# Kernel optimization log

Measured on AMD Instinct MI355X. Metric: run time of the kernel, lower is better.

The kernel has to match this reference:

```python
import jax, jax.numpy as jnp
import numpy as np

K = 16  # K_neighbors

def linear_positions(pixels):
    # normalized flat (pixels, 2) grid positions, matching LinearPositions(normalize=True, flat_output=True)
    wd = int(round(pixels ** 0.5))
    h = jnp.repeat(jnp.arange(wd, dtype=jnp.float32)[:, None], wd, axis=1)
    w = jnp.repeat(jnp.arange(wd, dtype=jnp.float32)[None, :], wd, axis=0)
    pos = jnp.stack([h, w], axis=-1) / (wd - 1)
    return pos.reshape(pixels, 2)


def setup_inputs() -> dict:
    key = jax.random.key(0)
    ks = jax.random.split(key, 8)
    B, Wn, P, C = 4, 16, 256, 32
    inp = {
        "x": jax.random.normal(ks[0], (B, Wn, P, C), dtype=jnp.float32),
        "sf_w0": jax.random.normal(ks[1], (3 * K, 128), dtype=jnp.float32) * 0.05,
        "sf_b0": jnp.zeros((128,), jnp.float32),
        "sf_w1": jax.random.normal(ks[2], (128, 128), dtype=jnp.float32) * 0.05,
        "sf_b1": jnp.zeros((128,), jnp.float32),
        "sf_wo": jax.random.normal(ks[3], (128, 64), dtype=jnp.float32) * 0.05,
        "sf_bo": jnp.zeros((64,), jnp.float32),
        "out_w0": jax.random.normal(ks[4], (C + 64, 128), dtype=jnp.float32) * 0.05,
        "out_b0": jnp.zeros((128,), jnp.float32),
        "out_w1": jax.random.normal(ks[5], (128, 128), dtype=jnp.float32) * 0.05,
        "out_b1": jnp.zeros((128,), jnp.float32),
        "out_wo": jax.random.normal(ks[6], (128, 64), dtype=jnp.float32) * 0.05,
        "out_bo": jnp.zeros((64,), jnp.float32),
    }
    return inp


def reference(x, sf_w0, sf_b0, sf_w1, sf_b1, sf_wo, sf_bo,
              out_w0, out_b0, out_w1, out_b1, out_wo, out_bo):
    B, Wn, P, C = x.shape
    # L1 similarity: 1 - mean |x_i - x_j| over channels -> (B, Wn, P, P)
    w = 1.0 - jnp.mean(jnp.abs(x[:, :, :, None, :] - x[:, :, None, :, :]), axis=-1)
    K_scores, K_idxs = jax.lax.top_k(w, K)  # (B, Wn, P, K)
    pos = linear_positions(P)  # (P, 2)
    # source pos for pixel i minus gathered target pos of its K neighbors
    rel = pos[None, None, :, None, :] - pos[K_idxs]  # (B, Wn, P, K, 2)
    K_rel_pos = rel.reshape(B, Wn, P, K * 2)
    # sf FFN
    h = jnp.concatenate([K_scores, K_rel_pos], axis=-1)  # (B, Wn, P, 3K)
    h = jax.nn.relu(h @ sf_w0 + sf_b0)
    h = jax.nn.relu(h @ sf_w1 + sf_b1)
    sf = h @ sf_wo + sf_bo  # (B, Wn, P, 64)
    # out FFN
    h = jnp.concatenate([x, sf], axis=-1)  # (B, Wn, P, C+64)
    h = jax.nn.relu(h @ out_w0 + out_b0)
    h = jax.nn.relu(h @ out_w1 + out_b1)
    return h @ out_wo + out_bo  # (B, Wn, P, 64)
```

## Files before the change

### kernel.cpp

```cpp
#include <hip/hip_runtime.h>
#include <hip/hip_bf16.h>

#define K_SEL 16
#define NCAND 20

typedef __attribute__((ext_vector_type(8))) short short8;
typedef __attribute__((ext_vector_type(4))) short short4v;
typedef __attribute__((ext_vector_type(4))) float f32x4;

__device__ __forceinline__ short f2bf_bits(float v) {
    union { __hip_bfloat16 b; short s; } u;
    u.b = __float2bfloat16(v);
    return u.s;
}
__device__ __forceinline__ float bf2f_bits(short h) {
    return __uint_as_float(((unsigned)(unsigned short)h) << 16);
}
__device__ __forceinline__ float readlane_f(float v, int l) {
    return __int_as_float(__builtin_amdgcn_readlane(__float_as_int(v), l));
}

__device__ __noinline__ void pack_body(
    int t,
    const float* __restrict__ s0w, const float* __restrict__ s1w,
    const float* __restrict__ sow, const float* __restrict__ o0w,
    const float* __restrict__ o1w, const float* __restrict__ oow,
    short* __restrict__ wpack)
{
    if (t >= 69632) return;
    int l, base;
    if      (t <  8192) { l = 0; base = 0;     }
    else if (t < 24576) { l = 1; base = 8192;  }
    else if (t < 32768) { l = 2; base = 24576; }
    else if (t < 45056) { l = 3; base = 32768; }
    else if (t < 61440) { l = 4; base = 45056; }
    else                { l = 5; base = 61440; }

    const float* W = (l == 0) ? s0w : (l == 1) ? s1w : (l == 2) ? sow
                   : (l == 3) ? o0w : (l == 4) ? o1w : oow;
    int N    = (l == 2 || l == 5) ? 64 : 128;
    int Kr   = (l == 0) ? 48 : (l == 3) ? 96 : 128;
    int woff = (l == 0) ? 0 : (l == 1) ? 16384 : (l == 2) ? 49152
             : (l == 3) ? 65536 : (l == 4) ? 90112 : 122880;
    int sz   = (l == 2 || l == 5) ? 8192 : (l == 3) ? 12288 : (l == 0) ? 8192 : 16384;

    int e = t - base;
    int i = e & 7, kb = (e >> 3) & 3, rem = e >> 5;
    int n = rem % N, ks = rem / N;
    int k = ks * 32 + kb * 8 + i;
    float v = (k < Kr) ? W[k * N + n] : 0.0f;
    short hi = f2bf_bits(v);
    float lo = v - bf2f_bits(hi);
    wpack[woff + e]      = hi;
    wpack[woff + sz + e] = f2bf_bits(lo);
}

template<int COMP>
__device__ __forceinline__ void simtopk_body(
    const float* __restrict__ x, float* __restrict__ feat,
    float* xsT, int* candj, double* rs, int win, int grp, int tid)
{
    const int lane = tid & 63;
    const int wv   = tid >> 6;

    if (tid < 512) {
        const int c4 = tid & 7, jb = tid >> 3;
        const float4* gx = reinterpret_cast<const float4*>(x + (size_t)win * 8192);
        float4 v0 = gx[jb * 8 + c4];
        float4 v1 = gx[jb * 8 + c4 + 512];
        float4 v2 = gx[jb * 8 + c4 + 1024];
        float4 v3 = gx[jb * 8 + c4 + 1536];
        float4* xsT4 = reinterpret_cast<float4*>(xsT);
        const int gsw = jb ^ c4;
        xsT4[(4 * c4 + 0) * 64 + gsw] = make_float4(v0.x, v1.x, v2.x, v3.x);
        xsT4[(4 * c4 + 1) * 64 + gsw] = make_float4(v0.y, v1.y, v2.y, v3.y);
        xsT4[(4 * c4 + 2) * 64 + gsw] = make_float4(v0.z, v1.z, v2.z, v3.z);
        xsT4[(4 * c4 + 3) * 64 + gsw] = make_float4(v0.w, v1.w, v2.w, v3.w);
    }
    __syncthreads();

    const int plbase = (grp & 1) * 32 + wv * 2;

    const f32x4* xsT4c = reinterpret_cast<const f32x4*>(xsT);
    float acc0[4] = {0.f, 0.f, 0.f, 0.f};
    float acc1[4] = {0.f, 0.f, 0.f, 0.f};
    #pragma unroll
    for (int c = 0; c < 32; ++c) {
        f32x4 a = xsT4c[c * 64 + (lane ^ ((c >> 2) & 7))];
        float xi0 = readlane_f(a[COMP], plbase);
        float xi1 = readlane_f(a[COMP], plbase + 1);
        #pragma unroll
        for (int q = 0; q < 4; ++q) {
            acc0[q] += fabsf(a[q] - xi0);
            acc1[q] += fabsf(a[q] - xi1);
        }
    }
    unsigned int p0[4], p1[4];
    #pragma unroll
    for (int q = 0; q < 4; ++q) {
        p0[q] = (__float_as_uint(acc0[q]) & 0xFFFFFF00u) | (unsigned)(q * 64 + lane);
        p1[q] = (__float_as_uint(acc1[q]) & 0xFFFFFF00u) | (unsigned)(q * 64 + lane);
    }

    unsigned int T0 = 0, T1 = 0;
    for (int bit = 31; bit >= 0; --bit) {
        unsigned int c0 = T0 | (1u << bit), c1 = T1 | (1u << bit);
        int n0 = __popcll(__ballot(p0[0] < c0)) + __popcll(__ballot(p0[1] < c0))
               + __popcll(__ballot(p0[2] < c0)) + __popcll(__ballot(p0[3] < c0));
        int n1 = __popcll(__ballot(p1[0] < c1)) + __popcll(__ballot(p1[1] < c1))
               + __popcll(__ballot(p1[2] < c1)) + __popcll(__ballot(p1[3] < c1));
        if (n0 < NCAND) T0 = c0;
        if (n1 < NCAND) T1 = c1;
    }

    const unsigned long long lt = (1ull << lane) - 1ull;
    int base0 = 0, base1 = 0;
    #pragma unroll
    for (int q = 0; q < 4; ++q) {
        bool s0 = (p0[q] <= T0);
        unsigned long long m0 = __ballot(s0);
        if (s0) candj[(wv * 2 + 0) * NCAND + base0 + __popcll(m0 & lt)] = q * 64 + lane;
        base0 += __popcll(m0);
        bool s1 = (p1[q] <= T1);
        unsigned long long m1 = __ballot(s1);
        if (s1) candj[(wv * 2 + 1) * NCAND + base1 + __popcll(m1 & lt)] = q * 64 + lane;
        base1 += __popcll(m1);
    }
    asm volatile("s_waitcnt lgkmcnt(0)" ::: "memory");

    const int t  = lane >> 5;
    const int cl = lane & 31;
    double s = 0.0;
    int myj = -1;
    if (cl < NCAND) {
        myj = candj[(wv * 2 + t) * NCAND + cl];
        const int pwin = COMP * 64 + plbase + t;
        const float4* xj = reinterpret_cast<const float4*>(x + (size_t)win * 8192 + (size_t)myj * 32);
        const float4* xp = reinterpret_cast<const float4*>(x + (size_t)win * 8192 + (size_t)pwin * 32);
        #pragma unroll
        for (int c4 = 0; c4 < 8; ++c4) {
            float4 b = xj[c4];
            float4 a = xp[c4];
            s += fabs((double)a.x - (double)b.x);
            s += fabs((double)a.y - (double)b.y);
            s += fabs((double)a.z - (double)b.z);
            s += fabs((double)a.w - (double)b.w);
        }
        rs[(wv * 2 + t) * NCAND + cl] = s;
    }
    asm volatile("s_waitcnt lgkmcnt(0)" ::: "memory");

    if (cl < NCAND) {
        int rank = 0;
        #pragma unroll 4
        for (int o = 0; o < NCAND; ++o) {
            double so = rs[(wv * 2 + t) * NCAND + o];
            int    jo = candj[(wv * 2 + t) * NCAND + o];
            rank += (so < s || (so == s && jo < myj)) ? 1 : 0;
        }
        if (rank < K_SEL) {
            const int pwin = COMP * 64 + plbase + t;
            const int gp   = win * 256 + pwin;
            feat[gp * 48 + rank] = (float)(1.0 - s * 0.03125);
            float dh = (float)((pwin >> 4) - (myj >> 4)) * (1.0f / 15.0f);
            float dw = (float)((pwin & 15) - (myj & 15)) * (1.0f / 15.0f);
            reinterpret_cast<float2*>(feat)[gp * 24 + 8 + rank] = make_float2(dh, dw);
        }
    }
}

__global__ __launch_bounds__(1024) void simtopk_kernel(
    const float* __restrict__ x,
    float* __restrict__ feat,
    const float* __restrict__ s0w, const float* __restrict__ s1w,
    const float* __restrict__ sow, const float* __restrict__ o0w,
    const float* __restrict__ o1w, const float* __restrict__ oow,
    short* __restrict__ wpack)
{
    __shared__ __align__(16) float xsT[8192];
    __shared__ int    candj[16 * 2 * NCAND];
    __shared__ double rs[16 * 2 * NCAND];

    const int tid = threadIdx.x;

    if (blockIdx.x >= 512) {
        pack_body((blockIdx.x - 512) * 1024 + tid,
                  s0w, s1w, sow, o0w, o1w, oow, wpack);
        return;
    }

    const int win = blockIdx.x >> 3;
    const int grp = blockIdx.x & 7;

    switch (grp >> 1) {
        case 0: simtopk_body<0>(x, feat, xsT, candj, rs, win, grp, tid); break;
        case 1: simtopk_body<1>(x, feat, xsT, candj, rs, win, grp, tid); break;
        case 2: simtopk_body<2>(x, feat, xsT, candj, rs, win, grp, tid); break;
        default: simtopk_body<3>(x, feat, xsT, candj, rs, win, grp, tid); break;
    }
}

template<int K_STEPS, int N, bool RELU, bool TO_GLOBAL>
__device__ __forceinline__ void bf16_layer64(
    const short* hiIn, const short* loIn, short* hiOut, short* loOut,
    float* gout, int pbase, const short* __restrict__ wpack, int woff, int sz,
    const float* __restrict__ bias, int wv, int lane, int out_col_off)
{
    const int nt   = (N == 128) ? wv : (wv & 3);
    const int mt0  = (N == 128) ? 0  : ((wv >> 2) * 2);
    const int MREP = (N == 128) ? 4  : 2;
    const int kb   = lane >> 4;
    const int n    = nt * 16 + (lane & 15);

    f32x4 acc[4];
    #pragma unroll
    for (int m = 0; m < 4; ++m) acc[m] = (f32x4){0.f, 0.f, 0.f, 0.f};

    #pragma unroll
    for (int ks = 0; ks < K_STEPS; ++ks) {
        const int wi = woff + ((ks * N + n) * 4 + kb) * 8;
        short8 whi = *(const short8*)(wpack + wi);
        short8 wlo = *(const short8*)(wpack + wi + sz);
        const int g = ks * 4 + kb;
        #pragma unroll
        for (int m = 0; m < MREP; ++m) {
            const int m_a = (mt0 + m) * 16 + (lane & 15);
            const int off = m_a * 256 + ((g ^ (m_a & 7)) << 4);
            short8 ahi = *(const short8*)((const char*)hiIn + off);
            short8 alo = *(const short8*)((const char*)loIn + off);
            acc[m] = __builtin_amdgcn_mfma_f32_16x16x32_bf16(ahi, whi, acc[m], 0, 0, 0);
            acc[m] = __builtin_amdgcn_mfma_f32_16x16x32_bf16(ahi, wlo, acc[m], 0, 0, 0);
            acc[m] = __builtin_amdgcn_mfma_f32_16x16x32_bf16(alo, whi, acc[m], 0, 0, 0);
        }
    }

    const float bv = bias[n];
    #pragma unroll
    for (int m = 0; m < MREP; ++m) {
        #pragma unroll
        for (int r = 0; r < 4; ++r) {
            float v = acc[m][r] + bv;
            if (RELU) v = fmaxf(v, 0.0f);
            const int pw = (mt0 + m) * 16 + (lane >> 4) * 4 + r;
            if (TO_GLOBAL) {
                gout[(size_t)(pbase + pw) * 64 + n] = v;
            } else {
                const int w   = out_col_off + n;
                const int off = pw * 256 + ((((w >> 3) ^ (pw & 7))) << 4) + (w & 7) * 2;
                short h = f2bf_bits(v);
                short l = f2bf_bits(v - bf2f_bits(h));
                *(short*)((char*)hiOut + off) = h;
                *(short*)((char*)loOut + off) = l;
            }
        }
    }
}

__global__ __launch_bounds__(512) void ffn_kernel(
    const float* __restrict__ x,
    const float* __restrict__ feat,
    const short* __restrict__ wpack,
    const float* __restrict__ s0b, const float* __restrict__ s1b,
    const float* __restrict__ sob, const float* __restrict__ o0b,
    const float* __restrict__ o1b, const float* __restrict__ oob,
    float* __restrict__ out)
{
    __shared__ __align__(16) short hiA[64 * 128];
    __shared__ __align__(16) short loA[64 * 128];
    __shared__ __align__(16) short hiB[64 * 128];
    __shared__ __align__(16) short loB[64 * 128];

    const int tid   = threadIdx.x;
    const int lane  = tid & 63;
    const int wv    = tid >> 6;
    const int pbase = blockIdx.x * 64;

    #pragma unroll
    for (int rr = 0; rr < 2; ++rr) {
        int u = tid + rr * 512;
        if (u < 768) {
            int p = u / 12, c4 = u - p * 12;
            f32x4 v = ((const f32x4*)feat)[(size_t)(pbase + p) * 12 + c4];
            short4v h4, l4;
            #pragma unroll
            for (int j = 0; j < 4; ++j) {
                short h = f2bf_bits(v[j]);
                h4[j] = h;
                l4[j] = f2bf_bits(v[j] - bf2f_bits(h));
            }
            int off = p * 256 + ((((c4 >> 1) ^ (p & 7))) << 4) + (c4 & 1) * 8;
            *(short4v*)((char*)hiA + off) = h4;
            *(short4v*)((char*)loA + off) = l4;
        }
    }
    if (tid < 256) {
        int p = tid >> 2, sel = tid & 3;
        int g = 6 + (sel & 1);
        int off = p * 256 + ((g ^ (p & 7)) << 4);
        short8 z = (short8){0,0,0,0,0,0,0,0};
        if (sel >> 1) *(short8*)((char*)loA + off) = z;
        else          *(short8*)((char*)hiA + off) = z;
    }
    __syncthreads();

    bf16_layer64<2, 128, true, false>(hiA, loA, hiB, loB, nullptr, pbase,
                                      wpack, 0, 8192, s0b, wv, lane, 0);
    __syncthreads();
    bf16_layer64<4, 128, true, false>(hiB, loB, hiA, loA, nullptr, pbase,
                                      wpack, 16384, 16384, s1b, wv, lane, 0);
    __syncthreads();
    {
        int p = tid >> 3, c4 = tid & 7;
        f32x4 v = ((const f32x4*)x)[(size_t)(pbase + p) * 8 + c4];
        short4v h4, l4;
        #pragma unroll
        for (int j = 0; j < 4; ++j) {
            short h = f2bf_bits(v[j]);
            h4[j] = h;
            l4[j] = f2bf_bits(v[j] - bf2f_bits(h));
        }
        int off = p * 256 + ((((c4 >> 1) ^ (p & 7))) << 4) + (c4 & 1) * 8;
        *(short4v*)((char*)hiB + off) = h4;
        *(short4v*)((char*)loB + off) = l4;
    }
    bf16_layer64<4, 64, false, false>(hiA, loA, hiB, loB, nullptr, pbase,
                                      wpack, 49152, 8192, sob, wv, lane, 32);
    __syncthreads();
    bf16_layer64<3, 128, true, false>(hiB, loB, hiA, loA, nullptr, pbase,
                                      wpack, 65536, 12288, o0b, wv, lane, 0);
    __syncthreads();
    bf16_layer64<4, 128, true, false>(hiA, loA, hiB, loB, nullptr, pbase,
                                      wpack, 90112, 16384, o1b, wv, lane, 0);
    __syncthreads();
    bf16_layer64<4, 64, false, true>(hiB, loB, nullptr, nullptr, out, pbase,
                                     wpack, 122880, 8192, oob, wv, lane, 0);
}

extern "C" void kernel_launch(void* const* d_in, const int* in_sizes, int n_in,
                              void* d_out, int out_size, void* d_ws, size_t ws_size,
                              hipStream_t stream) {
    const float* x    = (const float*)d_in[0];
    const float* s0w  = (const float*)d_in[1];
    const float* s0b  = (const float*)d_in[2];
    const float* s1w  = (const float*)d_in[3];
    const float* s1b  = (const float*)d_in[4];
    const float* sow  = (const float*)d_in[5];
    const float* sob  = (const float*)d_in[6];
    const float* o0w  = (const float*)d_in[7];
    const float* o0b  = (const float*)d_in[8];
    const float* o1w  = (const float*)d_in[9];
    const float* o1b  = (const float*)d_in[10];
    const float* oow  = (const float*)d_in[11];
    const float* oob  = (const float*)d_in[12];

    short* wpack = (short*)d_ws;
    float* feat  = (float*)((char*)d_ws + 524288);
    float* out   = (float*)d_out;

    simtopk_kernel<<<580, 1024, 0, stream>>>(x, feat,
                                             s0w, s1w, sow, o0w, o1w, oow, wpack);
    ffn_kernel<<<256, 512, 0, stream>>>(x, feat, wpack,
                                        s0b, s1b, sob, o0b, o1b, oob,
                                        out);
}
```

Measured before the change: 50.00 us.

## Halve simtopk block size, process four pixels per wave, use shuffles for ranking

Result: slower. 51.22 us (+2.4%).

```diff
diff --git a/kernel.cpp b/kernel.cpp
--- a/kernel.cpp
+++ b/kernel.cpp
@@ -58,12 +58,12 @@
 template<int COMP>
 __device__ __forceinline__ void simtopk_body(
     const float* __restrict__ x, float* __restrict__ feat,
-    float* xsT, int* candj, double* rs, int win, int grp, int tid)
+    float* xsT, int* candj, int win, int grp, int tid)
 {
     const int lane = tid & 63;
     const int wv   = tid >> 6;
 
-    if (tid < 512) {
+    {
         const int c4 = tid & 7, jb = tid >> 3;
         const float4* gx = reinterpret_cast<const float4*>(x + (size_t)win * 8192);
         float4 v0 = gx[jb * 8 + c4];
@@ -79,97 +79,137 @@
     }
     __syncthreads();
 
-    const int plbase = (grp & 1) * 32 + wv * 2;
+    const int plb = (grp & 1) * 32 + wv * 4;
 
     const f32x4* xsT4c = reinterpret_cast<const f32x4*>(xsT);
-    float acc0[4] = {0.f, 0.f, 0.f, 0.f};
-    float acc1[4] = {0.f, 0.f, 0.f, 0.f};
+    float acc0[4] = {0.f,0.f,0.f,0.f};
+    float acc1[4] = {0.f,0.f,0.f,0.f};
+    float acc2[4] = {0.f,0.f,0.f,0.f};
+    float acc3[4] = {0.f,0.f,0.f,0.f};
     #pragma unroll
     for (int c = 0; c < 32; ++c) {
         f32x4 a = xsT4c[c * 64 + (lane ^ ((c >> 2) & 7))];
-        float xi0 = readlane_f(a[COMP], plbase);
-        float xi1 = readlane_f(a[COMP], plbase + 1);
+        float xi0 = readlane_f(a[COMP], plb);
+        float xi1 = readlane_f(a[COMP], plb + 1);
+        float xi2 = readlane_f(a[COMP], plb + 2);
+        float xi3 = readlane_f(a[COMP], plb + 3);
         #pragma unroll
         for (int q = 0; q < 4; ++q) {
             acc0[q] += fabsf(a[q] - xi0);
             acc1[q] += fabsf(a[q] - xi1);
-        }
-    }
-    unsigned int p0[4], p1[4];
+            acc2[q] += fabsf(a[q] - xi2);
+            acc3[q] += fabsf(a[q] - xi3);
+        }
+    }
+    unsigned int p0[4], p1[4], p2[4], p3[4];
     #pragma unroll
     for (int q = 0; q < 4; ++q) {
-        p0[q] = (__float_as_uint(acc0[q]) & 0xFFFFFF00u) | (unsigned)(q * 64 + lane);
-        p1[q] = (__float_as_uint(acc1[q]) & 0xFFFFFF00u) | (unsigned)(q * 64 + lane);
-    }
-
-    unsigned int T0 = 0, T1 = 0;
+        unsigned idx = (unsigned)(q * 64 + lane);
+        p0[q] = (__float_as_uint(acc0[q]) & 0xFFFFFF00u) | idx;
+        p1[q] = (__float_as_uint(acc1[q]) & 0xFFFFFF00u) | idx;
+        p2[q] = (__float_as_uint(acc2[q]) & 0xFFFFFF00u) | idx;
+        p3[q] = (__float_as_uint(acc3[q]) & 0xFFFFFF00u) | idx;
+    }
+
+    unsigned int T0 = 0, T1 = 0, T2 = 0, T3 = 0;
     for (int bit = 31; bit >= 0; --bit) {
         unsigned int c0 = T0 | (1u << bit), c1 = T1 | (1u << bit);
+        unsigned int c2 = T2 | (1u << bit), c3 = T3 | (1u << bit);
         int n0 = __popcll(__ballot(p0[0] < c0)) + __popcll(__ballot(p0[1] < c0))
                + __popcll(__ballot(p0[2] < c0)) + __popcll(__ballot(p0[3] < c0));
         int n1 = __popcll(__ballot(p1[0] < c1)) + __popcll(__ballot(p1[1] < c1))
                + __popcll(__ballot(p1[2] < c1)) + __popcll(__ballot(p1[3] < c1));
+        int n2 = __popcll(__ballot(p2[0] < c2)) + __popcll(__ballot(p2[1] < c2))
+               + __popcll(__ballot(p2[2] < c2)) + __popcll(__ballot(p2[3] < c2));
+        int n3 = __popcll(__ballot(p3[0] < c3)) + __popcll(__ballot(p3[1] < c3))
+               + __popcll(__ballot(p3[2] < c3)) + __popcll(__ballot(p3[3] < c3));
         if (n0 < NCAND) T0 = c0;
         if (n1 < NCAND) T1 = c1;
+        if (n2 < NCAND) T2 = c2;
+        if (n3 < NCAND) T3 = c3;
     }
 
     const unsigned long long lt = (1ull << lane) - 1ull;
-    int base0 = 0, base1 = 0;
-    #pragma unroll
-    for (int q = 0; q < 4; ++q) {
-        bool s0 = (p0[q] <= T0);
-        unsigned long long m0 = __ballot(s0);
-        if (s0) candj[(wv * 2 + 0) * NCAND + base0 + __popcll(m0 & lt)] = q * 64 + lane;
-        base0 += __popcll(m0);
-        bool s1 = (p1[q] <= T1);
-        unsigned long long m1 = __ballot(s1);
-        if (s1) candj[(wv * 2 + 1) * NCAND + base1 + __popcll(m1 & lt)] = q * 64 + lane;
-        base1 += __popcll(m1);
+    {
+        int b0 = 0, b1 = 0, b2 = 0, b3 = 0;
+        #pragma unroll
+        for (int q = 0; q < 4; ++q) {
+            bool s0 = (p0[q] <= T0);
+            unsigned long long m0 = __ballot(s0);
+            if (s0) candj[(wv * 4 + 0) * NCAND + b0 + __popcll(m0 & lt)] = q * 64 + lane;
+            b0 += __popcll(m0);
+            bool s1 = (p1[q] <= T1);
+            unsigned long long m1 = __ballot(s1);
+            if (s1) candj[(wv * 4 + 1) * NCAND + b1 + __popcll(m1 & lt)] = q * 64 + lane;
+            b1 += __popcll(m1);
+            bool s2 = (p2[q] <= T2);
+            unsigned long long m2 = __ballot(s2);
+            if (s2) candj[(wv * 4 + 2) * NCAND + b2 + __popcll(m2 & lt)] = q * 64 + lane;
+            b2 += __popcll(m2);
+            bool s3 = (p3[q] <= T3);
+            unsigned long long m3 = __ballot(s3);
+            if (s3) candj[(wv * 4 + 3) * NCAND + b3 + __popcll(m3 & lt)] = q * 64 + lane;
+            b3 += __popcll(m3);
+        }
     }
     asm volatile("s_waitcnt lgkmcnt(0)" ::: "memory");
 
-    const int t  = lane >> 5;
+    const int th = lane >> 5;
     const int cl = lane & 31;
-    double s = 0.0;
-    int myj = -1;
+    const float* xw = x + (size_t)win * 8192;
+
+    double sA = 0.0, sB = 0.0;
+    int jA = -1, jB = -1;
     if (cl < NCAND) {
-        myj = candj[(wv * 2 + t) * NCAND + cl];
-        const int pwin = COMP * 64 + plbase + t;
-        const float4* xj = reinterpret_cast<const float4*>(x + (size_t)win * 8192 + (size_t)myj * 32);
-        const float4* xp = reinterpret_cast<const float4*>(x + (size_t)win * 8192 + (size_t)pwin * 32);
+        jA = candj[(wv * 4 + th) * NCAND + cl];
+        const float4* xj = reinterpret_cast<const float4*>(xw + (size_t)jA * 32);
+        const float4* xp = reinterpret_cast<const float4*>(xw + (size_t)(COMP * 64 + plb + th) * 32);
         #pragma unroll
         for (int c4 = 0; c4 < 8; ++c4) {
             float4 b = xj[c4];
             float4 a = xp[c4];
-            s += fabs((double)a.x - (double)b.x);
-            s += fabs((double)a.y - (double)b.y);
-            s += fabs((double)a.z - (double)b.z);
-            s += fabs((double)a.w - (double)b.w);
-        }
-        rs[(wv * 2 + t) * NCAND + cl] = s;
-    }
-    asm volatile("s_waitcnt lgkmcnt(0)" ::: "memory");
-
-    if (cl < NCAND) {
+            sA += fabs((double)a.x - (double)b.x);
+            sA += fabs((double)a.y - (double)b.y);
+            sA += fabs((double)a.z - (double)b.z);
+            sA += fabs((double)a.w - (double)b.w);
+        }
+        jB = candj[(wv * 4 + 2 + th) * NCAND + cl];
+        const float4* xj2 = reinterpret_cast<const float4*>(xw + (size_t)jB * 32);
+        const float4* xp2 = reinterpret_cast<const float4*>(xw + (size_t)(COMP * 64 + plb + 2 + th) * 32);
+        #pragma unroll
+        for (int c4 = 0; c4 < 8; ++c4) {
+            float4 b = xj2[c4];
+            float4 a = xp2[c4];
+            sB += fabs((double)a.x - (double)b.x);
+            sB += fabs((double)a.y - (double)b.y);
+            sB += fabs((double)a.z - (double)b.z);
+            sB += fabs((double)a.w - (double)b.w);
+        }
+    }
+
+    const int gbase = th * 32;
+    #pragma unroll 2
+    for (int r = 0; r < 2; ++r) {
+        double sm = (r == 0) ? sA : sB;
+        int    jm = (r == 0) ? jA : jB;
         int rank = 0;
-        #pragma unroll 4
         for (int o = 0; o < NCAND; ++o) {
-            double so = rs[(wv * 2 + t) * NCAND + o];
-            int    jo = candj[(wv * 2 + t) * NCAND + o];
-            rank += (so < s || (so == s && jo < myj)) ? 1 : 0;
-        }
-        if (rank < K_SEL) {
-            const int pwin = COMP * 64 + plbase + t;
+            double so = __shfl(sm, gbase + o, 64);
+            int    jo = __shfl(jm, gbase + o, 64);
+            rank += (so < sm || (so == sm && jo < jm)) ? 1 : 0;
+        }
+        if (cl < NCAND && rank < K_SEL) {
+            const int pwin = COMP * 64 + plb + r * 2 + th;
             const int gp   = win * 256 + pwin;
-            feat[gp * 48 + rank] = (float)(1.0 - s * 0.03125);
-            float dh = (float)((pwin >> 4) - (myj >> 4)) * (1.0f / 15.0f);
-            float dw = (float)((pwin & 15) - (myj & 15)) * (1.0f / 15.0f);
+            feat[gp * 48 + rank] = (float)(1.0 - sm * 0.03125);
+            float dh = (float)((pwin >> 4) - (jm >> 4)) * (1.0f / 15.0f);
+            float dw = (float)((pwin & 15) - (jm & 15)) * (1.0f / 15.0f);
             reinterpret_cast<float2*>(feat)[gp * 24 + 8 + rank] = make_float2(dh, dw);
         }
     }
 }
 
-__global__ __launch_bounds__(1024) void simtopk_kernel(
+__global__ __launch_bounds__(512) void simtopk_kernel(
     const float* __restrict__ x,
     float* __restrict__ feat,
     const float* __restrict__ s0w, const float* __restrict__ s1w,
@@ -178,13 +218,12 @@
     short* __restrict__ wpack)
 {
     __shared__ __align__(16) float xsT[8192];
-    __shared__ int    candj[16 * 2 * NCAND];
-    __shared__ double rs[16 * 2 * NCAND];
+    __shared__ int candj[8 * 4 * NCAND];
 
     const int tid = threadIdx.x;
 
     if (blockIdx.x >= 512) {
-        pack_body((blockIdx.x - 512) * 1024 + tid,
+        pack_body((blockIdx.x - 512) * 512 + tid,
                   s0w, s1w, sow, o0w, o1w, oow, wpack);
         return;
     }
@@ -193,10 +232,10 @@
     const int grp = blockIdx.x & 7;
 
     switch (grp >> 1) {
-        case 0: simtopk_body<0>(x, feat, xsT, candj, rs, win, grp, tid); break;
-        case 1: simtopk_body<1>(x, feat, xsT, candj, rs, win, grp, tid); break;
-        case 2: simtopk_body<2>(x, feat, xsT, candj, rs, win, grp, tid); break;
-        default: simtopk_body<3>(x, feat, xsT, candj, rs, win, grp, tid); break;
+        case 0: simtopk_body<0>(x, feat, xsT, candj, win, grp, tid); break;
+        case 1: simtopk_body<1>(x, feat, xsT, candj, win, grp, tid); break;
+        case 2: simtopk_body<2>(x, feat, xsT, candj, win, grp, tid); break;
+        default: simtopk_body<3>(x, feat, xsT, candj, win, grp, tid); break;
     }
 }
 
@@ -357,8 +396,8 @@
     float* feat  = (float*)((char*)d_ws + 524288);
     float* out   = (float*)d_out;
 
-    simtopk_kernel<<<580, 1024, 0, stream>>>(x, feat,
-                                             s0w, s1w, sow, o0w, o1w, oow, wpack);
+    simtopk_kernel<<<648, 512, 0, stream>>>(x, feat,
+                                            s0w, s1w, sow, o0w, o1w, oow, wpack);
     ffn_kernel<<<256, 512, 0, stream>>>(x, feat, wpack,
                                         s0b, s1b, sob, o0b, o1b, oob,
                                         out);
```
